# Performance work log

Measured on AMD Instinct MI355X. Metric: run time of the kernel, lower is better.

The kernel has to match this reference:

```python
import jax, jax.numpy as jnp
import numpy as np

DIM = 1024
HEADS = 16


def setup_inputs() -> dict:
    key = jax.random.key(0)
    ks = jax.random.split(key, 8)
    b, n, d = 2, 2048, DIM
    x = jax.random.normal(ks[0], (b, n, d), dtype=jnp.float32)
    # Linear(dim, 3*dim, bias=False): weight stored as [dim, 3*dim] (pre-transposed)
    W_qkv = jax.random.normal(ks[1], (d, 3 * d), dtype=jnp.float32) * (d ** -0.5)
    # Linear(dim, dim) with bias
    W_out = jax.random.normal(ks[2], (d, d), dtype=jnp.float32) * (d ** -0.5)
    b_out = jnp.zeros((d,), dtype=jnp.float32)
    alpha = jnp.ones((1,), dtype=jnp.float32)
    beta = jnp.zeros((1,), dtype=jnp.float32) + 0.5  # nonzero so softmax path is exercised
    gamma = jnp.zeros((1,), dtype=jnp.float32) + 0.1
    return {"x": x, "W_qkv": W_qkv, "W_out": W_out, "b_out": b_out,
            "alpha": alpha, "beta": beta, "gamma": gamma}


def reference(x, W_qkv, W_out, b_out, alpha, beta, gamma):
    b, n, d = x.shape
    h = HEADS
    hd = d // h
    scale = d ** -0.5  # note: full dim, as in the original module
    qkv = x @ W_qkv  # [b, n, 3d]
    q, k, v = jnp.split(qkv, 3, axis=-1)
    # [b, n, d] -> [b, h, n, hd]
    to_heads = lambda t: t.reshape(b, n, h, hd).transpose(0, 2, 1, 3)
    q, k, v = to_heads(q), to_heads(k), to_heads(v)
    dots = jnp.einsum("bhqd,bhkd->bhqk", q, k) * scale  # [b, h, n, n]
    attn = (alpha[0] * jnp.eye(n, dtype=x.dtype)
            + beta[0] * jax.nn.softmax(dots, axis=-1)
            - gamma[0] / n)
    out = jnp.einsum("bhqk,bhkd->bhqd", attn, v)  # [b, h, n, hd]
    out = out.transpose(0, 2, 1, 3).reshape(b, n, d)
    return out @ W_out + b_out
```

## Files before the change

### kernel.cpp

```cpp
#include <hip/hip_runtime.h>
#include <hip/hip_bf16.h>

#define DEVI __device__ __forceinline__

typedef __attribute__((ext_vector_type(8))) short bf16x8;
typedef __attribute__((ext_vector_type(4))) short bf16x4;
typedef __attribute__((ext_vector_type(4))) float f32x4;

DEVI unsigned short f2bf(float f) {
    unsigned u = __float_as_uint(f);
    u += 0x7FFF + ((u >> 16) & 1);
    return (unsigned short)(u >> 16);
}
DEVI float bf2f(unsigned short h) {
    return __uint_as_float(((unsigned)h) << 16);
}
DEVI f32x4 mfma16(bf16x8 a, bf16x8 b, f32x4 c) {
    return __builtin_amdgcn_mfma_f32_16x16x32_bf16(a, b, c, 0, 0, 0);
}
DEVI void gload_lds16(const void* g, void* l) {
    __builtin_amdgcn_global_load_lds(
        (const __attribute__((address_space(1))) unsigned int*)g,
        (__attribute__((address_space(3))) unsigned int*)l, 16, 0, 0);
}

DEVI void wt_body(const float* __restrict__ W, unsigned short* __restrict__ Wt,
                  int N, int n0, int k0, float sc, int tid,
                  unsigned short (*T)[72])
{
#pragma unroll
    for (int j = 0; j < 4; ++j) {
        int idx = tid + j * 256;
        int kk = idx >> 4, c4 = (idx & 15) << 2;
        float4 v = *(const float4*)(W + (size_t)(k0 + kk) * N + n0 + c4);
        T[c4 + 0][kk] = f2bf(v.x * sc); T[c4 + 1][kk] = f2bf(v.y * sc);
        T[c4 + 2][kk] = f2bf(v.z * sc); T[c4 + 3][kk] = f2bf(v.w * sc);
    }
    __syncthreads();
#pragma unroll
    for (int j = 0; j < 4; ++j) {
        int idx = tid + j * 256;
        int n = idx >> 4, c4 = (idx & 15) << 2;
        *(bf16x4*)(Wt + (size_t)(n0 + n) * 1024 + k0 + c4) = *(bf16x4*)&T[n][c4];
    }
}

__global__ __launch_bounds__(256) void k_prep(
    const float* __restrict__ X, const float* __restrict__ Wqkv,
    const float* __restrict__ Wout,
    unsigned short* __restrict__ Xb, unsigned short* __restrict__ Wt1,
    unsigned short* __restrict__ Wt2, float* __restrict__ vsum)
{
    __shared__ unsigned short T[64][72];
    const int tid = threadIdx.x;
    const int bid = blockIdx.x;
    const float QSC = 1.4426950408889634f / 32.0f;
    if (bid < 1024) {
        if (bid == 0) {
            float4 z = (float4){0.f, 0.f, 0.f, 0.f};
            ((float4*)vsum)[tid] = z;
            ((float4*)vsum)[tid + 256] = z;
        }
        int i = bid * 256 + tid;
#pragma unroll
        for (int j = 0; j < 4; ++j) {
            int idx = i + j * 262144;
            float4 v = *(const float4*)(X + (size_t)idx * 4);
            bf16x4 hv;
            hv[0] = (short)f2bf(v.x); hv[1] = (short)f2bf(v.y);
            hv[2] = (short)f2bf(v.z); hv[3] = (short)f2bf(v.w);
            *(bf16x4*)(Xb + (size_t)idx * 4) = hv;
        }
    } else if (bid < 1792) {
        int idx = bid - 1024;
        int n0 = (idx % 48) * 64, k0 = (idx / 48) * 64;
        wt_body(Wqkv, Wt1, 3072, n0, k0, (n0 < 1024) ? QSC : 1.0f, tid, T);
    } else {
        int idx = bid - 1792;
        int n0 = (idx & 15) * 64, k0 = (idx >> 4) * 64;
        wt_body(Wout, Wt2, 1024, n0, k0, 1.0f, tid, T);
    }
}

__global__ __launch_bounds__(256) void k_gemm1(
    const unsigned short* __restrict__ A, const unsigned short* __restrict__ B,
    unsigned short* __restrict__ C, unsigned short* __restrict__ Vt,
    float* __restrict__ vsum)
{
    __shared__ unsigned short Sh[32768];
    const int tid = threadIdx.x, lane = tid & 63, wid = tid >> 6;
    const int wr = (wid >> 1) * 64, wc = (wid & 1) * 64;
    const int row0 = blockIdx.y * 128, col0 = (23 - blockIdx.x) * 128;
    const int rsel = lane & 15, kgr = (lane >> 4) * 8;
    const int lr = lane >> 3, lc = (lane & 7) * 8;

    f32x4 acc[4][4];
#pragma unroll
    for (int i = 0; i < 4; ++i)
#pragma unroll
        for (int j = 0; j < 4; ++j) acc[i][j] = (f32x4){0.f, 0.f, 0.f, 0.f};

    const unsigned short* ap[4];
    const unsigned short* bp[4];
#pragma unroll
    for (int i = 0; i < 4; ++i) {
        ap[i] = A + (size_t)(row0 + wid * 32 + i * 8 + lr) * 1024 + lc;
        bp[i] = B + (size_t)(col0 + wid * 32 + i * 8 + lr) * 1024 + lc;
    }

#define GSTAGE(BUF)                                                            \
    {                                                                          \
        _Pragma("unroll")                                                      \
        for (int i = 0; i < 4; ++i) {                                          \
            int rb = wid * 32 + i * 8;                                         \
            gload_lds16(ap[i], Sh + (BUF) * 16384 + rb * 64);                  \
            gload_lds16(bp[i], Sh + (BUF) * 16384 + 8192 + rb * 64);           \
            ap[i] += 64; bp[i] += 64;                                          \
        }                                                                      \
    }

#define GCOMP(CUR)                                                             \
    {                                                                          \
        const unsigned short* As_ = Sh + (CUR) * 16384;                        \
        const unsigned short* Bs_ = As_ + 8192;                                \
        _Pragma("unroll")                                                      \
        for (int ks = 0; ks < 2; ++ks) {                                       \
            bf16x8 a[4], b[4];                                                 \
            int ko = ks * 32 + kgr;                                            \
            _Pragma("unroll")                                                  \
            for (int mi = 0; mi < 4; ++mi)                                     \
                a[mi] = *(const bf16x8*)(As_ + (wr + mi * 16 + rsel) * 64 + ko);\
            _Pragma("unroll")                                                  \
            for (int nj = 0; nj < 4; ++nj)                                     \
                b[nj] = *(const bf16x8*)(Bs_ + (wc + nj * 16 + rsel) * 64 + ko);\
            _Pragma("unroll")                                                  \
            for (int mi = 0; mi < 4; ++mi)                                     \
                _Pragma("unroll")                                              \
                for (int nj = 0; nj < 4; ++nj)                                 \
                    acc[mi][nj] = mfma16(a[mi], b[nj], acc[mi][nj]);           \
        }                                                                      \
    }

#define GBODY(CUR, DOPF)                                                       \
    {                                                                          \
        if (DOPF) GSTAGE((CUR) ^ 1);                                           \
        GCOMP(CUR);                                                            \
        asm volatile("s_waitcnt vmcnt(0)" ::: "memory");                       \
        __syncthreads();                                                       \
    }

    GSTAGE(0);
    asm volatile("s_waitcnt vmcnt(0)" ::: "memory");
    __syncthreads();
#pragma unroll 1
    for (int i = 0; i < 8; ++i) {
        GBODY(0, true);
        GBODY(1, (i < 7));
    }
#undef GBODY
#undef GCOMP
#undef GSTAGE

    __syncthreads();
    unsigned short (*wb)[72] = (unsigned short (*)[72])(Sh + wid * 4608);
    const int g4 = (lane >> 4) << 2;
#pragma unroll
    for (int mi = 0; mi < 4; ++mi)
#pragma unroll
        for (int nj = 0; nj < 4; ++nj)
#pragma unroll
            for (int r = 0; r < 4; ++r)
                wb[mi * 16 + g4 + r][nj * 16 + rsel] = f2bf(acc[mi][nj][r]);
#pragma unroll
    for (int rr = 0; rr < 8; ++rr) {
        int row = rr * 8 + (lane >> 3);
        int c8 = (lane & 7) * 8;
        bf16x8 v = *(const bf16x8*)&wb[row][c8];
        *(bf16x8*)(C + (size_t)(row0 + wr + row) * 3072 + col0 + wc + c8) = v;
    }

    if (col0 >= 2048) {
        const int b_ = row0 >> 11;
        const int n0 = (row0 & 2047) + wr;
        const int bh = b_ * 16 + ((col0 + wc - 2048) >> 6);
#pragma unroll
        for (int nj = 0; nj < 4; ++nj) {
            float s = 0.f;
#pragma unroll
            for (int mi = 0; mi < 4; ++mi)
#pragma unroll
                for (int r = 0; r < 4; ++r) s += acc[mi][nj][r];
            s += __shfl_xor(s, 16);
            s += __shfl_xor(s, 32);
            if (lane < 16) atomicAdd(&vsum[bh * 64 + nj * 16 + rsel], s);
        }
        unsigned short* vtb = Vt + (size_t)bh * 64 * 2048 + n0 + lane;
#pragma unroll 8
        for (int dv = 0; dv < 64; ++dv)
            vtb[(size_t)dv * 2048] = wb[lane][dv];
    }
}

__global__ __launch_bounds__(256) void k_attn(
    const unsigned short* __restrict__ qkv, const unsigned short* __restrict__ Vt,
    const float* __restrict__ vsum,
    const float* __restrict__ alpha_p, const float* __restrict__ beta_p,
    const float* __restrict__ gamma_p,
    unsigned short* __restrict__ AO)
{
    __shared__ unsigned short Ks[4][64][64];
    __shared__ unsigned short Vs[4][64][64];
    __shared__ unsigned short Ps[4][32][64];
    const int tid = threadIdx.x, lane = tid & 63, wid = tid >> 6;
    const int swz = (blockIdx.x & 7) * 64 + (blockIdx.x >> 3);
    const int bh = swz >> 4, qtb = swz & 15;
    const int b = bh >> 4, h = bh & 15;
    const int q0 = qtb * 128;
    const int rsel = lane & 15, g = lane >> 4;
    const int g4 = g << 2;
    const int wq0 = wid * 32;
    const int r7 = rsel & 7;

    bf16x8 bq[2][2];
#pragma unroll
    for (int qt = 0; qt < 2; ++qt) {
        const unsigned short* qrow =
            qkv + (size_t)(b * 2048 + q0 + wq0 + qt * 16 + rsel) * 3072 + h * 64;
        bq[qt][0] = *(const bf16x8*)(qrow + g * 8);
        bq[qt][1] = *(const bf16x8*)(qrow + 32 + g * 8);
    }

    const int sr = lane >> 3;
    const int ss = (lane & 7) ^ sr;
    const int rb0 = wid * 16, rb1 = wid * 16 + 8;
    const unsigned short* kp0 = qkv + (size_t)(b * 2048) * 3072 + 1024 + h * 64
                              + (size_t)(rb0 + sr) * 3072 + ss * 8;
    const unsigned short* kp1 = kp0 + (size_t)8 * 3072;
    const unsigned short* vp0 = Vt + (size_t)bh * 64 * 2048
                              + (size_t)(rb0 + sr) * 2048 + ss * 8;
    const unsigned short* vp1 = vp0 + (size_t)8 * 2048;
    const size_t KADV = (size_t)64 * 3072;

    f32x4 o[2][4], ol[2];
#pragma unroll
    for (int qt = 0; qt < 2; ++qt) {
#pragma unroll
        for (int dj = 0; dj < 4; ++dj) o[qt][dj] = (f32x4){0.f, 0.f, 0.f, 0.f};
        ol[qt] = (f32x4){0.f, 0.f, 0.f, 0.f};
    }
    bf16x8 ones;
#pragma unroll
    for (int e = 0; e < 8; ++e) ones[e] = (short)0x3F80;

#define STAGE(BUF)                                                             \
    {                                                                          \
        gload_lds16(kp0, &Ks[BUF][rb0][0]);                                    \
        gload_lds16(kp1, &Ks[BUF][rb1][0]);                                    \
        gload_lds16(vp0, &Vs[BUF][rb0][0]);                                    \
        gload_lds16(vp1, &Vs[BUF][rb1][0]);                                    \
        kp0 += KADV; kp1 += KADV; vp0 += 64; vp1 += 64;                        \
    }

    STAGE(0); STAGE(1);
    asm volatile("s_waitcnt vmcnt(0)" ::: "memory");
    __syncthreads();

#define QK(CUR, S)                                                             \
    {                                                                          \
        _Pragma("unroll")                                                      \
        for (int qt = 0; qt < 2; ++qt)                                         \
            _Pragma("unroll")                                                  \
            for (int kj = 0; kj < 4; ++kj)                                     \
                S[qt][kj] = (f32x4){0.f, 0.f, 0.f, 0.f};                       \
        __builtin_amdgcn_s_setprio(1);                                         \
        _Pragma("unroll")                                                      \
        for (int ks = 0; ks < 2; ++ks) {                                       \
            const int sl = ((ks * 4 + g) ^ r7) * 8;                            \
            bf16x8 ak[4];                                                      \
            _Pragma("unroll")                                                  \
            for (int kj = 0; kj < 4; ++kj)                                     \
                ak[kj] = *(const bf16x8*)(&Ks[CUR][kj * 16 + rsel][sl]);       \
            _Pragma("unroll")                                                  \
            for (int qt = 0; qt < 2; ++qt)                                     \
                _Pragma("unroll")                                              \
                for (int kj = 0; kj < 4; ++kj)                                 \
                    S[qt][kj] = mfma16(ak[kj], bq[qt][ks], S[qt][kj]);         \
        }                                                                      \
        __builtin_amdgcn_s_setprio(0);                                         \
    }

#define EPV(CUR, S)                                                            \
    {                                                                          \
        _Pragma("unroll")                                                      \
        for (int qt = 0; qt < 2; ++qt)                                         \
            _Pragma("unroll")                                                  \
            for (int kj = 0; kj < 4; ++kj) {                                   \
                float p0 = __builtin_amdgcn_exp2f(S[qt][kj][0]);               \
                float p1 = __builtin_amdgcn_exp2f(S[qt][kj][1]);               \
                float p2 = __builtin_amdgcn_exp2f(S[qt][kj][2]);               \
                float p3 = __builtin_amdgcn_exp2f(S[qt][kj][3]);               \
                union { __hip_bfloat162 h2[2]; uint2 u; } pk;                  \
                pk.h2[0] = __float22bfloat162_rn(make_float2(p0, p1));         \
                pk.h2[1] = __float22bfloat162_rn(make_float2(p2, p3));         \
                const int slot16 = (kj * 2 + (g >> 1)) ^ r7;                   \
                *(uint2*)(&Ps[wid][qt * 16 + rsel][slot16 * 8 + (g & 1) * 4])  \
                    = pk.u;                                                    \
            }                                                                  \
        __builtin_amdgcn_s_setprio(1);                                         \
        _Pragma("unroll")                                                      \
        for (int ks = 0; ks < 2; ++ks) {                                       \
            const int sl = ((ks * 4 + g) ^ r7) * 8;                            \
            bf16x8 pa0 = *(const bf16x8*)(&Ps[wid][rsel][sl]);                 \
            bf16x8 pa1 = *(const bf16x8*)(&Ps[wid][16 + rsel][sl]);            \
            bf16x8 vb[4];                                                      \
            _Pragma("unroll")                                                  \
            for (int dj = 0; dj < 4; ++dj)                                     \
                vb[dj] = *(const bf16x8*)(&Vs[CUR][dj * 16 + rsel][sl]);       \
            _Pragma("unroll")                                                  \
            for (int dj = 0; dj < 4; ++dj) {                                   \
                o[0][dj] = mfma16(pa0, vb[dj], o[0][dj]);                      \
                o[1][dj] = mfma16(pa1, vb[dj], o[1][dj]);                      \
            }                                                                  \
            ol[0] = mfma16(pa0, ones, ol[0]);                                  \
            ol[1] = mfma16(pa1, ones, ol[1]);                                  \
        }                                                                      \
        __builtin_amdgcn_s_setprio(0);                                         \
    }

#define PAIR(C0, C1, DOPF)                                                     \
    {                                                                          \
        f32x4 s0[2][4], s1[2][4];                                              \
        if (DOPF) { STAGE(C0 ^ 2); STAGE(C1 ^ 2); }                            \
        QK(C0, s0);                                                            \
        QK(C1, s1);                                                            \
        EPV(C0, s0);                                                           \
        EPV(C1, s1);                                                           \
        asm volatile("s_waitcnt vmcnt(0)" ::: "memory");                       \
        __syncthreads();                                                       \
    }

#pragma unroll 1
    for (int i = 0; i < 8; ++i) {
        PAIR(0, 1, true);
        PAIR(2, 3, (i < 7));
    }
#undef PAIR
#undef EPV
#undef QK
#undef STAGE

    const float alpha = *alpha_p, beta = *beta_p;
    const float gn = (*gamma_p) / 2048.0f;
#pragma unroll
    for (int qt = 0; qt < 2; ++qt) {
        float linv[4];
#pragma unroll
        for (int r = 0; r < 4; ++r)
            linv[r] = beta / ol[qt][r];
#pragma unroll
        for (int dj = 0; dj < 4; ++dj)
#pragma unroll
            for (int r = 0; r < 4; ++r) {
                int qrow = q0 + wq0 + qt * 16 + g4 + r;
                int dv = dj * 16 + rsel;
                float ov = o[qt][dj][r] * linv[r];
                float vdiag = bf2f(qkv[(size_t)(b * 2048 + qrow) * 3072 + 2048 + h * 64 + dv]);
                float vs = vsum[bh * 64 + dv];
                float res = ov + alpha * vdiag - gn * vs;
                AO[(size_t)(b * 2048 + qrow) * 1024 + h * 64 + dv] = f2bf(res);
            }
    }
}

__global__ __launch_bounds__(256) void k_gemm2(
    const unsigned short* __restrict__ A, const unsigned short* __restrict__ B,
    const float* __restrict__ bias, float* __restrict__ Out)
{
    __shared__ unsigned short Sh[16384];
    const int tid = threadIdx.x, lane = tid & 63, wid = tid >> 6;
    const int wr = (wid >> 1) * 32, wc = (wid & 1) * 32;
    const int row0 = blockIdx.y * 64, col0 = blockIdx.x * 64;
    const int rsel = lane & 15, kgr = (lane >> 4) * 8;
    const int lr = lane >> 3, lc = (lane & 7) * 8;

    f32x4 acc[2][2];
#pragma unroll
    for (int i = 0; i < 2; ++i)
#pragma unroll
        for (int j = 0; j < 2; ++j) acc[i][j] = (f32x4){0.f, 0.f, 0.f, 0.f};

    const unsigned short* ap[2];
    const unsigned short* bp[2];
#pragma unroll
    for (int i = 0; i < 2; ++i) {
        ap[i] = A + (size_t)(row0 + wid * 16 + i * 8 + lr) * 1024 + lc;
        bp[i] = B + (size_t)(col0 + wid * 16 + i * 8 + lr) * 1024 + lc;
    }

#define G2STAGE(BUF)                                                           \
    {                                                                          \
        _Pragma("unroll")                                                      \
        for (int i = 0; i < 2; ++i) {                                          \
            int rb = wid * 16 + i * 8;                                         \
            gload_lds16(ap[i], Sh + (BUF) * 8192 + rb * 64);                   \
            gload_lds16(bp[i], Sh + (BUF) * 8192 + 4096 + rb * 64);            \
            ap[i] += 64; bp[i] += 64;                                          \
        }                                                                      \
    }

#define G2BODY(CUR, DOPF)                                                      \
    {                                                                          \
        if (DOPF) G2STAGE((CUR) ^ 1);                                          \
        const unsigned short* As_ = Sh + (CUR) * 8192;                         \
        const unsigned short* Bs_ = As_ + 4096;                                \
        _Pragma("unroll")                                                      \
        for (int ks = 0; ks < 2; ++ks) {                                       \
            bf16x8 a[2], b[2];                                                 \
            int ko = ks * 32 + kgr;                                            \
            _Pragma("unroll")                                                  \
            for (int mi = 0; mi < 2; ++mi)                                     \
                a[mi] = *(const bf16x8*)(As_ + (wr + mi * 16 + rsel) * 64 + ko);\
            _Pragma("unroll")                                                  \
            for (int nj = 0; nj < 2; ++nj)                                     \
                b[nj] = *(const bf16x8*)(Bs_ + (wc + nj * 16 + rsel) * 64 + ko);\
            _Pragma("unroll")                                                  \
            for (int mi = 0; mi < 2; ++mi)                                     \
                _Pragma("unroll")                                              \
                for (int nj = 0; nj < 2; ++nj)                                 \
                    acc[mi][nj] = mfma16(a[mi], b[nj], acc[mi][nj]);           \
        }                                                                      \
        asm volatile("s_waitcnt vmcnt(0)" ::: "memory");                       \
        __syncthreads();                                                       \
    }

    G2STAGE(0);
    asm volatile("s_waitcnt vmcnt(0)" ::: "memory");
    __syncthreads();
#pragma unroll 1
    for (int i = 0; i < 8; ++i) {
        G2BODY(0, true);
        G2BODY(1, (i < 7));
    }
#undef G2BODY
#undef G2STAGE

    const int rbase = row0 + wr + ((lane >> 4) << 2);
    const int cbase = col0 + wc + rsel;
#pragma unroll
    for (int mi = 0; mi < 2; ++mi)
#pragma unroll
        for (int nj = 0; nj < 2; ++nj) {
            int gc = cbase + nj * 16;
            float bv = bias[gc];
#pragma unroll
            for (int r = 0; r < 4; ++r)
                Out[(size_t)(rbase + mi * 16 + r) * 1024 + gc] = acc[mi][nj][r] + bv;
        }
}

extern "C" void kernel_launch(void* const* d_in, const int* in_sizes, int n_in,
                              void* d_out, int out_size, void* d_ws, size_t ws_size,
                              hipStream_t stream) {
    const float* x     = (const float*)d_in[0];
    const float* Wqkv  = (const float*)d_in[1];
    const float* Wout  = (const float*)d_in[2];
    const float* bout  = (const float*)d_in[3];
    const float* alpha = (const float*)d_in[4];
    const float* beta  = (const float*)d_in[5];
    const float* gamma = (const float*)d_in[6];
    float* out = (float*)d_out;

    char* ws = (char*)d_ws;
    unsigned short* Xb  = (unsigned short*)(ws);
    unsigned short* Wt1 = (unsigned short*)(ws + 8388608);
    unsigned short* Wt2 = (unsigned short*)(ws + 14680064);
    unsigned short* qkv = (unsigned short*)(ws + 16777216);
    unsigned short* Vt  = (unsigned short*)(ws + 41943040);
    float* vsum         = (float*)(ws + 50331648);
    unsigned short* AO  = Xb;

    k_prep<<<2048, 256, 0, stream>>>(x, Wqkv, Wout, Xb, Wt1, Wt2, vsum);
    k_gemm1<<<dim3(24, 32), 256, 0, stream>>>(Xb, Wt1, qkv, Vt, vsum);
    k_attn<<<512, 256, 0, stream>>>(qkv, Vt, vsum, alpha, beta, gamma, AO);
    k_gemm2<<<dim3(16, 64), 256, 0, stream>>>(AO, Wt2, bout, out);
}
```

Baseline: 122.1 us.

## Use 32x32 MFMA with transposed scores and register-resident P via permlane swap

Restructures the attention inner loop to use 32x32x16 bf16 MFMAs and computes S transposed (K as A operand, Q as B), so each lane holds one query's scores. The probability tile stays in registers and is rearranged with v_permlane32_swap instead of a round trip through LDS, and the row sum is accumulated directly from the fp32 exps instead of an extra MFMA against a ones vector. The epilogue now writes vectorized 4-element bf16 chunks per query row. This removes the Ps shared buffer, its LDS writes and reads, and the extra MFMA work, at the cost of depending on a gfx950-specific permlane instruction and a correct operand layout.

```diff
diff --git a/kernel.cpp b/kernel.cpp
--- a/kernel.cpp
+++ b/kernel.cpp
@@ -6,6 +6,7 @@
 typedef __attribute__((ext_vector_type(8))) short bf16x8;
 typedef __attribute__((ext_vector_type(4))) short bf16x4;
 typedef __attribute__((ext_vector_type(4))) float f32x4;
+typedef __attribute__((ext_vector_type(16))) float f32x16;
 
 DEVI unsigned short f2bf(float f) {
     unsigned u = __float_as_uint(f);
@@ -17,6 +18,9 @@
 }
 DEVI f32x4 mfma16(bf16x8 a, bf16x8 b, f32x4 c) {
     return __builtin_amdgcn_mfma_f32_16x16x32_bf16(a, b, c, 0, 0, 0);
+}
+DEVI f32x16 mfma32(bf16x8 a, bf16x8 b, f32x16 c) {
+    return __builtin_amdgcn_mfma_f32_32x32x16_bf16(a, b, c, 0, 0, 0);
 }
 DEVI void gload_lds16(const void* g, void* l) {
     __builtin_amdgcn_global_load_lds(
@@ -210,24 +214,20 @@
 {
     __shared__ unsigned short Ks[4][64][64];
     __shared__ unsigned short Vs[4][64][64];
-    __shared__ unsigned short Ps[4][32][64];
     const int tid = threadIdx.x, lane = tid & 63, wid = tid >> 6;
     const int swz = (blockIdx.x & 7) * 64 + (blockIdx.x >> 3);
     const int bh = swz >> 4, qtb = swz & 15;
     const int b = bh >> 4, h = bh & 15;
     const int q0 = qtb * 128;
-    const int rsel = lane & 15, g = lane >> 4;
-    const int g4 = g << 2;
-    const int wq0 = wid * 32;
-    const int r7 = rsel & 7;
-
-    bf16x8 bq[2][2];
-#pragma unroll
-    for (int qt = 0; qt < 2; ++qt) {
-        const unsigned short* qrow =
-            qkv + (size_t)(b * 2048 + q0 + wq0 + qt * 16 + rsel) * 3072 + h * 64;
-        bq[qt][0] = *(const bf16x8*)(qrow + g * 8);
-        bq[qt][1] = *(const bf16x8*)(qrow + 32 + g * 8);
+    const int l31 = lane & 31, hi = lane >> 5, l7 = lane & 7;
+    const int qrow = q0 + wid * 32 + l31;
+
+    bf16x8 qb[4];
+    {
+        const unsigned short* qptr = qkv + (size_t)(b * 2048 + qrow) * 3072 + h * 64;
+#pragma unroll
+        for (int ks = 0; ks < 4; ++ks)
+            qb[ks] = *(const bf16x8*)(qptr + ks * 16 + hi * 8);
     }
 
     const int sr = lane >> 3;
@@ -241,16 +241,8 @@
     const unsigned short* vp1 = vp0 + (size_t)8 * 2048;
     const size_t KADV = (size_t)64 * 3072;
 
-    f32x4 o[2][4], ol[2];
-#pragma unroll
-    for (int qt = 0; qt < 2; ++qt) {
-#pragma unroll
-        for (int dj = 0; dj < 4; ++dj) o[qt][dj] = (f32x4){0.f, 0.f, 0.f, 0.f};
-        ol[qt] = (f32x4){0.f, 0.f, 0.f, 0.f};
-    }
-    bf16x8 ones;
-#pragma unroll
-    for (int e = 0; e < 8; ++e) ones[e] = (short)0x3F80;
+    f32x16 o0 = (f32x16)0.f, o1 = (f32x16)0.f;
+    float lsum = 0.f;
 
 #define STAGE(BUF)                                                             \
     {                                                                          \
@@ -265,76 +257,73 @@
     asm volatile("s_waitcnt vmcnt(0)" ::: "memory");
     __syncthreads();
 
-#define QK(CUR, S)                                                             \
-    {                                                                          \
-        _Pragma("unroll")                                                      \
-        for (int qt = 0; qt < 2; ++qt)                                         \
-            _Pragma("unroll")                                                  \
-            for (int kj = 0; kj < 4; ++kj)                                     \
-                S[qt][kj] = (f32x4){0.f, 0.f, 0.f, 0.f};                       \
+#define TILE(CUR)                                                              \
+    {                                                                          \
+        f32x16 s0_ = (f32x16)0.f, s1_ = (f32x16)0.f;                           \
         __builtin_amdgcn_s_setprio(1);                                         \
         _Pragma("unroll")                                                      \
-        for (int ks = 0; ks < 2; ++ks) {                                       \
-            const int sl = ((ks * 4 + g) ^ r7) * 8;                            \
-            bf16x8 ak[4];                                                      \
-            _Pragma("unroll")                                                  \
-            for (int kj = 0; kj < 4; ++kj)                                     \
-                ak[kj] = *(const bf16x8*)(&Ks[CUR][kj * 16 + rsel][sl]);       \
-            _Pragma("unroll")                                                  \
-            for (int qt = 0; qt < 2; ++qt)                                     \
-                _Pragma("unroll")                                              \
-                for (int kj = 0; kj < 4; ++kj)                                 \
-                    S[qt][kj] = mfma16(ak[kj], bq[qt][ks], S[qt][kj]);         \
+        for (int ks = 0; ks < 4; ++ks) {                                       \
+            const int sl = (((ks << 1) | hi) ^ l7) * 8;                        \
+            bf16x8 ak0 = *(const bf16x8*)(&Ks[CUR][l31][sl]);                  \
+            bf16x8 ak1 = *(const bf16x8*)(&Ks[CUR][32 + l31][sl]);             \
+            s0_ = mfma32(ak0, qb[ks], s0_);                                    \
+            s1_ = mfma32(ak1, qb[ks], s1_);                                    \
         }                                                                      \
         __builtin_amdgcn_s_setprio(0);                                         \
-    }
-
-#define EPV(CUR, S)                                                            \
-    {                                                                          \
-        _Pragma("unroll")                                                      \
-        for (int qt = 0; qt < 2; ++qt)                                         \
-            _Pragma("unroll")                                                  \
-            for (int kj = 0; kj < 4; ++kj) {                                   \
-                float p0 = __builtin_amdgcn_exp2f(S[qt][kj][0]);               \
-                float p1 = __builtin_amdgcn_exp2f(S[qt][kj][1]);               \
-                float p2 = __builtin_amdgcn_exp2f(S[qt][kj][2]);               \
-                float p3 = __builtin_amdgcn_exp2f(S[qt][kj][3]);               \
-                union { __hip_bfloat162 h2[2]; uint2 u; } pk;                  \
-                pk.h2[0] = __float22bfloat162_rn(make_float2(p0, p1));         \
-                pk.h2[1] = __float22bfloat162_rn(make_float2(p2, p3));         \
-                const int slot16 = (kj * 2 + (g >> 1)) ^ r7;                   \
-                *(uint2*)(&Ps[wid][qt * 16 + rsel][slot16 * 8 + (g & 1) * 4])  \
-                    = pk.u;                                                    \
-            }                                                                  \
+        unsigned w0[2][4], w1[2][4];                                           \
+        _Pragma("unroll")                                                      \
+        for (int j = 0; j < 4; ++j) {                                          \
+            float p0 = __builtin_amdgcn_exp2f(s0_[4 * j + 0]);                 \
+            float p1 = __builtin_amdgcn_exp2f(s0_[4 * j + 1]);                 \
+            float p2 = __builtin_amdgcn_exp2f(s0_[4 * j + 2]);                 \
+            float p3 = __builtin_amdgcn_exp2f(s0_[4 * j + 3]);                 \
+            lsum += (p0 + p1) + (p2 + p3);                                     \
+            union { __hip_bfloat162 h2; unsigned u; } k0_, k1_;                \
+            k0_.h2 = __float22bfloat162_rn(make_float2(p0, p1));               \
+            k1_.h2 = __float22bfloat162_rn(make_float2(p2, p3));               \
+            w0[0][j] = k0_.u; w1[0][j] = k1_.u;                                \
+        }                                                                      \
+        _Pragma("unroll")                                                      \
+        for (int j = 0; j < 4; ++j) {                                          \
+            float p0 = __builtin_amdgcn_exp2f(s1_[4 * j + 0]);                 \
+            float p1 = __builtin_amdgcn_exp2f(s1_[4 * j + 1]);                 \
+            float p2 = __builtin_amdgcn_exp2f(s1_[4 * j + 2]);                 \
+            float p3 = __builtin_amdgcn_exp2f(s1_[4 * j + 3]);                 \
+            lsum += (p0 + p1) + (p2 + p3);                                     \
+            union { __hip_bfloat162 h2; unsigned u; } k0_, k1_;                \
+            k0_.h2 = __float22bfloat162_rn(make_float2(p0, p1));               \
+            k1_.h2 = __float22bfloat162_rn(make_float2(p2, p3));               \
+            w0[1][j] = k0_.u; w1[1][j] = k1_.u;                                \
+        }                                                                      \
+        bf16x8 pb[4];                                                          \
+        _Pragma("unroll")                                                      \
+        for (int ks = 0; ks < 4; ++ks) {                                       \
+            const int t = ks >> 1, jj = (ks & 1) * 2;                          \
+            unsigned A_ = w0[t][jj], B_ = w0[t][jj + 1];                       \
+            unsigned C_ = w1[t][jj], D_ = w1[t][jj + 1];                       \
+            asm volatile("v_permlane32_swap_b32 %0, %1" : "+v"(A_), "+v"(B_)); \
+            asm volatile("v_permlane32_swap_b32 %0, %1" : "+v"(C_), "+v"(D_)); \
+            union { unsigned u[4]; bf16x8 v; } f_;                             \
+            f_.u[0] = A_; f_.u[1] = C_; f_.u[2] = B_; f_.u[3] = D_;            \
+            pb[ks] = f_.v;                                                     \
+        }                                                                      \
         __builtin_amdgcn_s_setprio(1);                                         \
         _Pragma("unroll")                                                      \
-        for (int ks = 0; ks < 2; ++ks) {                                       \
-            const int sl = ((ks * 4 + g) ^ r7) * 8;                            \
-            bf16x8 pa0 = *(const bf16x8*)(&Ps[wid][rsel][sl]);                 \
-            bf16x8 pa1 = *(const bf16x8*)(&Ps[wid][16 + rsel][sl]);            \
-            bf16x8 vb[4];                                                      \
-            _Pragma("unroll")                                                  \
-            for (int dj = 0; dj < 4; ++dj)                                     \
-                vb[dj] = *(const bf16x8*)(&Vs[CUR][dj * 16 + rsel][sl]);       \
-            _Pragma("unroll")                                                  \
-            for (int dj = 0; dj < 4; ++dj) {                                   \
-                o[0][dj] = mfma16(pa0, vb[dj], o[0][dj]);                      \
-                o[1][dj] = mfma16(pa1, vb[dj], o[1][dj]);                      \
-            }                                                                  \
-            ol[0] = mfma16(pa0, ones, ol[0]);                                  \
-            ol[1] = mfma16(pa1, ones, ol[1]);                                  \
+        for (int ks = 0; ks < 4; ++ks) {                                       \
+            const int sl = (((ks << 1) | hi) ^ l7) * 8;                        \
+            bf16x8 av0 = *(const bf16x8*)(&Vs[CUR][l31][sl]);                  \
+            bf16x8 av1 = *(const bf16x8*)(&Vs[CUR][32 + l31][sl]);             \
+            o0 = mfma32(av0, pb[ks], o0);                                      \
+            o1 = mfma32(av1, pb[ks], o1);                                      \
         }                                                                      \
         __builtin_amdgcn_s_setprio(0);                                         \
     }
 
 #define PAIR(C0, C1, DOPF)                                                     \
     {                                                                          \
-        f32x4 s0[2][4], s1[2][4];                                              \
         if (DOPF) { STAGE(C0 ^ 2); STAGE(C1 ^ 2); }                            \
-        QK(C0, s0);                                                            \
-        QK(C1, s1);                                                            \
-        EPV(C0, s0);                                                           \
-        EPV(C1, s1);                                                           \
+        TILE(C0);                                                              \
+        TILE(C1);                                                              \
         asm volatile("s_waitcnt vmcnt(0)" ::: "memory");                       \
         __syncthreads();                                                       \
     }
@@ -345,31 +334,32 @@
         PAIR(2, 3, (i < 7));
     }
 #undef PAIR
-#undef EPV
-#undef QK
+#undef TILE
 #undef STAGE
+
+    const float ltot = lsum + __shfl_xor(lsum, 32);
 
     const float alpha = *alpha_p, beta = *beta_p;
     const float gn = (*gamma_p) / 2048.0f;
-#pragma unroll
-    for (int qt = 0; qt < 2; ++qt) {
-        float linv[4];
-#pragma unroll
-        for (int r = 0; r < 4; ++r)
-            linv[r] = beta / ol[qt][r];
-#pragma unroll
-        for (int dj = 0; dj < 4; ++dj)
+    const float linv = beta / ltot;
+    const unsigned short* vrow = qkv + (size_t)(b * 2048 + qrow) * 3072 + 2048 + h * 64;
+    unsigned short* arow = AO + (size_t)(b * 2048 + qrow) * 1024 + h * 64;
+#pragma unroll
+    for (int t = 0; t < 2; ++t)
+#pragma unroll
+        for (int j = 0; j < 4; ++j) {
+            const int dv0 = t * 32 + 8 * j + 4 * hi;
+            bf16x4 vd = *(const bf16x4*)(vrow + dv0);
+            f32x4 vs = *(const f32x4*)(vsum + bh * 64 + dv0);
+            bf16x4 outp;
 #pragma unroll
             for (int r = 0; r < 4; ++r) {
-                int qrow = q0 + wq0 + qt * 16 + g4 + r;
-                int dv = dj * 16 + rsel;
-                float ov = o[qt][dj][r] * linv[r];
-                float vdiag = bf2f(qkv[(size_t)(b * 2048 + qrow) * 3072 + 2048 + h * 64 + dv]);
-                float vs = vsum[bh * 64 + dv];
-                float res = ov + alpha * vdiag - gn * vs;
-                AO[(size_t)(b * 2048 + qrow) * 1024 + h * 64 + dv] = f2bf(res);
+                float ov = (t == 0) ? o0[4 * j + r] : o1[4 * j + r];
+                float res = ov * linv + alpha * bf2f((unsigned short)vd[r]) - gn * vs[r];
+                outp[r] = (short)f2bf(res);
             }
-    }
+            *(bf16x4*)(arow + dv0) = outp;
+        }
 }
 
 __global__ __launch_bounds__(256) void k_gemm2(
```

Measured after the change: 124.1 us. About the same (+1.6%).
